# Optimization experiments

Measured on AMD Instinct MI355X. Metric: run time of the kernel, lower is better.

The kernel has to match this reference:

```python
import jax, jax.numpy as jnp
import numpy as np

B, S, D, L = 4, 4096, 2048, 4
QH, KVH, WINDOW = 16, 4, 512
HD = D // QH
G = QH // KVH
CAPF = 0.25
EPS = float(jnp.finfo(jnp.float32).eps)  # torch RMSNorm default eps for fp32


def setup_inputs() -> dict:
    key = jax.random.key(0)
    ks = jax.random.split(key, 8)
    s = 0.02
    return {
        "x": jax.random.normal(ks[0], (B, S, D), jnp.float32),
        "router_w": jax.random.normal(ks[1], (1, D), jnp.float32) * s,
        "norm1_w": jnp.ones((L, D), jnp.float32),
        "norm2_w": jnp.ones((L, D), jnp.float32),
        "qkv_w": jax.random.normal(ks[2], (L, (QH + 2 * KVH) * HD, D), jnp.float32) * s,
        "proj_w": jax.random.normal(ks[3], (L, D, D), jnp.float32) * s,
        "fc1_w": jax.random.normal(ks[4], (L, 2 * D, D), jnp.float32) * s,
        "fc2_w": jax.random.normal(ks[5], (L, D, D), jnp.float32) * s,
    }


def rmsnorm(x, w):
    return x * jax.lax.rsqrt(jnp.mean(x * x, -1, keepdims=True) + EPS) * w


def gqa(x, qkv_w, proj_w):
    # x: [B, C, D]; causal sliding-window attention with ALiBi (flash_attn semantics)
    b, c, _ = x.shape
    qkv = x @ qkv_w.T
    q = qkv[..., : QH * HD].reshape(b, c, KVH, G, HD)
    k = qkv[..., QH * HD:(QH + KVH) * HD].reshape(b, c, KVH, HD)
    v = qkv[..., (QH + KVH) * HD:].reshape(b, c, KVH, HD)
    scale = 1.0 / np.sqrt(HD)
    scores = jnp.einsum('bqkgd,bskd->bkgqs', q, k) * scale  # [B,KVH,G,C,C]
    i = jnp.arange(c)[:, None]
    j = jnp.arange(c)[None, :]
    diff = (i - j).astype(jnp.float32)
    mask = (diff >= 0) & (diff <= WINDOW)  # causal + left window
    slopes = jnp.exp2(-((jnp.arange(QH, dtype=jnp.float32) + 1.0) * 8.0 / QH))
    slopes = slopes.reshape(KVH, G, 1, 1)  # q head h = kvh*G + g ordering
    scores = jnp.where(mask, scores - slopes * diff, -jnp.inf)
    p = jax.nn.softmax(scores, axis=-1)
    att = jnp.einsum('bkgqs,bskd->bqkgd', p, v).reshape(b, c, QH * HD)
    return att @ proj_w.T


def swiglu(x, fc1_w, fc2_w):
    h = x @ fc1_w.T
    a, gate = jnp.split(h, 2, axis=-1)
    return (jax.nn.silu(gate) * a) @ fc2_w.T


def reference(x, router_w, norm1_w, norm2_w, qkv_w, proj_w, fc1_w, fc2_w):
    b, s, d = x.shape
    rw = jax.nn.sigmoid(x @ router_w.T)  # [B, S, 1]
    cap = int(s * CAPF)  # training path: capacity = int(seq_len * capacity_factor)
    rws = rw[..., 0]
    _, top_idx = jax.lax.top_k(rws, cap)            # unsorted-by-position top-k
    idx_sorted = jnp.sort(top_idx, axis=1)          # restore sequence order
    order = jnp.argsort(top_idx, axis=1)
    # faithful to source: gathers router_weights at the sort-order permutation
    # indices (values in [0, cap)), exactly as torch.gather(router_weights, 1, router_top_order)
    top_w = jnp.take_along_axis(rws, order, axis=1)[..., None]  # [B, cap, 1]
    lat = jnp.take_along_axis(x, idx_sorted[..., None], axis=1)  # [B, cap, D]
    for l in range(L):
        lat = lat + gqa(rmsnorm(lat, norm1_w[l]), qkv_w[l], proj_w[l])
        lat = lat + swiglu(rmsnorm(lat, norm2_w[l]), fc1_w[l], fc2_w[l])
    lat = lat * top_w
    bidx = jnp.arange(b)[:, None]
    pred = jnp.zeros_like(x).at[bidx, idx_sorted].set(lat)
    decisions = jnp.zeros_like(rw).at[bidx, idx_sorted].set(1.0)
    return pred, rw, decisions
```

## Files before the change

kernel.cpp:

```cpp
#include <hip/hip_runtime.h>
#include <hip/hip_bf16.h>

constexpr int NB = 4;
constexpr int SEQ = 4096;
constexpr int DIM = 2048;
constexpr int NLAYER = 4;
constexpr int NQH = 16;
constexpr int NKVH = 4;
constexpr int WIN = 512;
constexpr int HDIM = 128;
constexpr int CAPN = 1024;
constexpr int MTOK = NB * CAPN;
constexpr int QKVN = (NQH + 2 * NKVH) * HDIM;
constexpr int VOFF = DIM + NKVH * HDIM;
constexpr float EPSF = 1.1920928955078125e-07f;

typedef __hip_bfloat16 bf16;
typedef __bf16 b16x8 __attribute__((ext_vector_type(8)));
typedef __bf16 b16x4 __attribute__((ext_vector_type(4)));
typedef float f32x4 __attribute__((ext_vector_type(4)));

#define MFMA16(a, b, c) __builtin_amdgcn_mfma_f32_16x16x32_bf16((a), (b), (c), 0, 0, 0)

__device__ __forceinline__ void gload_lds16(const void* g, void* l) {
  __builtin_amdgcn_global_load_lds((__attribute__((address_space(1))) void*)(void*)g,
                                   (__attribute__((address_space(3))) void*)l, 16, 0, 0);
}

__global__ __launch_bounds__(256) void cast_kernel(const float* __restrict__ in,
                                                   bf16* __restrict__ out, int n) {
  int i = (blockIdx.x * 256 + threadIdx.x) * 4;
  if (i >= n) return;
  float4 v = *(const float4*)(in + i);
  b16x4 o;
  o[0] = (__bf16)v.x; o[1] = (__bf16)v.y; o[2] = (__bf16)v.z; o[3] = (__bf16)v.w;
  *(b16x4*)((__bf16*)out + i) = o;
}

__global__ __launch_bounds__(256) void cast_fc1_kernel(const float* __restrict__ in,
                                                       bf16* __restrict__ out) {
  int p = blockIdx.x;
  int chunk = p >> 5, w = p & 31;
  int L = (w < 16) ? (chunk * 16 + w) : (DIM + chunk * 16 + (w - 16));
  const float4* spv = (const float4*)(in + (size_t)L * DIM);
  __bf16* op = (__bf16*)out + (size_t)p * DIM;
  int t = threadIdx.x;
#pragma unroll
  for (int j = 0; j < 2; ++j) {
    float4 v = spv[t + j * 256];
    b16x4 o;
    o[0] = (__bf16)v.x; o[1] = (__bf16)v.y; o[2] = (__bf16)v.z; o[3] = (__bf16)v.w;
    *(b16x4*)(op + (t + j * 256) * 4) = o;
  }
}

__global__ __launch_bounds__(256) void router_kernel(const float* __restrict__ x,
                                                     const float* __restrict__ rwt,
                                                     float* __restrict__ rw_out) {
  int tok = blockIdx.x * 4 + (threadIdx.x >> 6);
  int l = threadIdx.x & 63;
  const float* xr = x + (size_t)tok * DIM;
  float s = 0.f;
  for (int c = l; c < DIM; c += 64) s += xr[c] * rwt[c];
  for (int off = 32; off; off >>= 1) s += __shfl_down(s, off);
  if (l == 0) rw_out[tok] = 1.f / (1.f + expf(-s));
}

__global__ __launch_bounds__(256) void rankcnt_kernel(const float* __restrict__ rw,
                                                      int* __restrict__ rank) {
  int blk = blockIdx.x;
  int ic = blk & 15, jc = (blk >> 4) & 15, b = blk >> 8;
  __shared__ float4 svi[64];
  int t = threadIdx.x;
  if (t < 64) svi[t] = ((const float4*)(rw + (size_t)b * SEQ + ic * 256))[t];
  __syncthreads();
  int j = jc * 256 + t;
  float vj = rw[(size_t)b * SEQ + j];
  int r = 0;
#pragma unroll 16
  for (int q = 0; q < 64; ++q) {
    float4 v = svi[q];
    int i = ic * 256 + q * 4;
    r += (v.x > vj || (v.x == vj && (i + 0) < j)) ? 1 : 0;
    r += (v.y > vj || (v.y == vj && (i + 1) < j)) ? 1 : 0;
    r += (v.z > vj || (v.z == vj && (i + 2) < j)) ? 1 : 0;
    r += (v.w > vj || (v.w == vj && (i + 3) < j)) ? 1 : 0;
  }
  atomicAdd(&rank[b * SEQ + j], r);
}

__global__ __launch_bounds__(1024) void select_kernel(const int* __restrict__ rank,
                                                      const float* __restrict__ rw,
                                                      int* __restrict__ idxs,
                                                      float* __restrict__ topw,
                                                      float* __restrict__ dec) {
  int b = blockIdx.x;
  int t = threadIdx.x;
  __shared__ int sr[SEQ];
  __shared__ int scnt[1024];
  for (int i = t; i < SEQ; i += 1024) sr[i] = rank[b * SEQ + i];
  __syncthreads();
  for (int i = t; i < SEQ; i += 1024) dec[(size_t)b * SEQ + i] = (sr[i] < CAPN) ? 1.0f : 0.0f;
  int c = 0;
#pragma unroll
  for (int k = 0; k < 4; ++k) c += (sr[t * 4 + k] < CAPN) ? 1 : 0;
  scnt[t] = c;
  __syncthreads();
  for (int off = 1; off < 1024; off <<= 1) {
    int v = scnt[t];
    int vm = (t >= off) ? scnt[t - off] : 0;
    __syncthreads();
    scnt[t] = v + vm;
    __syncthreads();
  }
  int pos = scnt[t] - c;
  for (int k = 0; k < 4; ++k) {
    int j = t * 4 + k;
    int r = sr[j];
    if (r < CAPN) {
      idxs[b * CAPN + pos] = j;
      topw[b * CAPN + pos] = rw[(size_t)b * SEQ + r];
      pos++;
    }
  }
}

__global__ __launch_bounds__(256) void gather_kernel(const float* __restrict__ x,
                                                     const int* __restrict__ idxs,
                                                     float* __restrict__ lat) {
  int tok = blockIdx.x;
  int b = tok >> 10, i = tok & 1023;
  int src = idxs[b * CAPN + i];
  const float4* spv = (const float4*)(x + ((size_t)b * SEQ + src) * DIM);
  float4* dp = (float4*)(lat + (size_t)tok * DIM);
  int t = threadIdx.x;
  dp[t] = spv[t];
  dp[t + 256] = spv[t + 256];
}

__global__ __launch_bounds__(256) void rmsnorm_kernel(const float* __restrict__ in,
                                                      const float* __restrict__ w,
                                                      bf16* __restrict__ out) {
  int row = blockIdx.x;
  int t = threadIdx.x;
  const float4* spv = (const float4*)(in + (size_t)row * DIM);
  float4 v0 = spv[t], v1 = spv[t + 256];
  float ss = v0.x * v0.x + v0.y * v0.y + v0.z * v0.z + v0.w * v0.w +
             v1.x * v1.x + v1.y * v1.y + v1.z * v1.z + v1.w * v1.w;
  for (int off = 32; off; off >>= 1) ss += __shfl_down(ss, off);
  __shared__ float red[4];
  if ((t & 63) == 0) red[t >> 6] = ss;
  __syncthreads();
  float total = red[0] + red[1] + red[2] + red[3];
  float sc = rsqrtf(total * (1.0f / DIM) + EPSF);
  const float4* wp = (const float4*)w;
  float4 w0 = wp[t], w1 = wp[t + 256];
  __bf16* op = (__bf16*)out + (size_t)row * DIM;
  b16x4 o0, o1;
  o0[0] = (__bf16)(v0.x * w0.x * sc); o0[1] = (__bf16)(v0.y * w0.y * sc);
  o0[2] = (__bf16)(v0.z * w0.z * sc); o0[3] = (__bf16)(v0.w * w0.w * sc);
  o1[0] = (__bf16)(v1.x * w1.x * sc); o1[1] = (__bf16)(v1.y * w1.y * sc);
  o1[2] = (__bf16)(v1.z * w1.z * sc); o1[3] = (__bf16)(v1.w * w1.w * sc);
  *(b16x4*)(op + t * 4) = o0;
  *(b16x4*)(op + 1024 + t * 4) = o1;
}


__device__ __forceinline__ void stage97(const bf16* g, int K, int kt,
                                        bf16* tile, int tid) {
#pragma unroll
  for (int j = 0; j < 4; ++j) {
    int q = j * 4096 + tid * 16;
    int row = q >> 7;
    int sc = ((tid & 7) ^ (row & 7)) << 3;
    gload_lds16((const __bf16*)g + (size_t)row * K + kt * 64 + sc,
                (char*)tile + q);
  }
}

__device__ __forceinline__ b16x8 frag97(const bf16* buf, int row, int ks, int hi) {
  int co = (ks * 32 + hi * 8) ^ ((row & 7) << 3);
  return *(const b16x8*)((const __bf16*)buf + row * 64 + co);
}

template <int MODE>
__global__ __launch_bounds__(256, 3) void gemm97(const bf16* __restrict__ A,
                                                 const bf16* __restrict__ Bw,
                                                 float* __restrict__ Cf,
                                                 bf16* __restrict__ Cb,
                                                 bf16* __restrict__ vTout,
                                                 int N, int K, int nbn) {
  __shared__ __align__(16) bf16 sA[128 * 64];
  __shared__ __align__(16) bf16 sB[128 * 64];
  const int tid = threadIdx.x;
  const int w = tid >> 6, l = tid & 63;
  const int lo = l & 15, hi = l >> 4;
  const int wr = w >> 1, wc = w & 1;
  const int nwg = gridDim.x;
  int bid = blockIdx.x;
  bid = (bid & 7) * (nwg >> 3) + (bid >> 3);
  const int bm = bid / nbn, bn = bid % nbn;
  const bf16* Ab = A + (size_t)bm * 128 * K;
  const bf16* Bb = Bw + (size_t)bn * 128 * K;
  const int nt = K >> 6;

  f32x4 acc[4][4];
#pragma unroll
  for (int i = 0; i < 4; ++i)
#pragma unroll
    for (int j = 0; j < 4; ++j) acc[i][j] = f32x4{0.f, 0.f, 0.f, 0.f};

  for (int t = 0; t < nt; ++t) {
    stage97(Ab, K, t, sA, tid);
    stage97(Bb, K, t, sB, tid);
    __syncthreads();
#pragma unroll
    for (int ks = 0; ks < 2; ++ks) {
      b16x8 af[4], bfm[4];
#pragma unroll
      for (int mi = 0; mi < 4; ++mi)
        af[mi] = frag97(sA, wr * 64 + mi * 16 + lo, ks, hi);
#pragma unroll
      for (int ni = 0; ni < 4; ++ni)
        bfm[ni] = frag97(sB, wc * 64 + ni * 16 + lo, ks, hi);
#pragma unroll
      for (int mi = 0; mi < 4; ++mi)
#pragma unroll
        for (int ni = 0; ni < 4; ++ni)
          acc[mi][ni] = MFMA16(af[mi], bfm[ni], acc[mi][ni]);
    }
    __syncthreads();
  }

#pragma unroll
  for (int mi = 0; mi < 4; ++mi) {
    int row0 = bm * 128 + wr * 64 + mi * 16 + hi * 4;
    if constexpr (MODE == 2) {
#pragma unroll
      for (int j2 = 0; j2 < 2; ++j2) {
        int colL = bn * 64 + wc * 32 + j2 * 16 + lo;
#pragma unroll
        for (int r = 0; r < 4; ++r) {
          float a = acc[mi][2 * j2][r];
          float g = acc[mi][2 * j2 + 1][r];
          float s = g / (1.f + __expf(-g));
          Cb[(size_t)(row0 + r) * DIM + colL] = __float2bfloat16(a * s);
        }
      }
    } else {
#pragma unroll
      for (int ni = 0; ni < 4; ++ni) {
        int col = bn * 128 + wc * 64 + ni * 16 + lo;
#pragma unroll
        for (int r = 0; r < 4; ++r) {
          size_t idx = (size_t)(row0 + r) * N + col;
          float v = acc[mi][ni][r];
          if constexpr (MODE == 3) {
            Cf[idx] += v;
          } else {
            bf16 bv = __float2bfloat16(v);
            Cb[idx] = bv;
            if constexpr (MODE == 1) {
              if (col >= VOFF) {
                int cc = col - VOFF;
                int kvh = cc >> 7, d = cc & 127;
                int row = row0 + r;
                int bb = row >> 10, tk = row & 1023;
                vTout[((size_t)(bb * NKVH + kvh) * HDIM + d) * CAPN + tk] = bv;
              }
            }
          }
        }
      }
    }
  }
}

__global__ __launch_bounds__(256) void attn_kernel(const bf16* __restrict__ qkvb,
                                                   const bf16* __restrict__ vT,
                                                   bf16* __restrict__ attb) {
  const int blk = blockIdx.x;
  const int qc = blk & 31;
  const int kvh = (blk >> 5) & 3;
  const int b = blk >> 7;
  const int w = threadIdx.x >> 6, l = threadIdx.x & 63;
  const int lo = l & 15, hi = l >> 4;
  const int h = kvh * 4 + w;
  const float slope = exp2f(-0.5f * (float)(h + 1));
  const float scale = 0.08838834764831845f;
  __shared__ __align__(16) bf16 p_lds[4][2][16 * 32];
  const __bf16* qp = (const __bf16*)qkvb;
  const __bf16* vtp = (const __bf16*)vT + (size_t)(b * NKVH + kvh) * HDIM * CAPN;
  const size_t tb = (size_t)b * CAPN;
  const int i0b = qc * 32;

  b16x8 aq[2][4];
#pragma unroll
  for (int qt = 0; qt < 2; ++qt) {
    const __bf16* qrow = qp + (tb + i0b + qt * 16 + lo) * QKVN + h * HDIM + hi * 8;
#pragma unroll
    for (int c = 0; c < 4; ++c) aq[qt][c] = *(const b16x8*)(qrow + c * 32);
  }

  f32x4 acc[2][8];
#pragma unroll
  for (int qt = 0; qt < 2; ++qt)
#pragma unroll
    for (int d = 0; d < 8; ++d) acc[qt][d] = f32x4{0.f, 0.f, 0.f, 0.f};
  float mrow[2][4], ssum[2][4];
#pragma unroll
  for (int qt = 0; qt < 2; ++qt)
#pragma unroll
    for (int r = 0; r < 4; ++r) { mrow[qt][r] = -1e30f; ssum[qt][r] = 0.f; }

  int jlo = i0b - WIN;
  if (jlo < 0) jlo = 0;
  jlo &= ~31;
  for (int j0 = jlo; j0 <= i0b; j0 += 32) {
    b16x8 kf[2][4];
#pragma unroll
    for (int jt = 0; jt < 2; ++jt) {
      const __bf16* krow = qp + (tb + j0 + jt * 16 + lo) * QKVN + DIM + kvh * HDIM + hi * 8;
#pragma unroll
      for (int c = 0; c < 4; ++c) kf[jt][c] = *(const b16x8*)(krow + c * 32);
    }
    f32x4 s[2][2];
#pragma unroll
    for (int qt = 0; qt < 2; ++qt)
#pragma unroll
      for (int jt = 0; jt < 2; ++jt) {
        s[qt][jt] = f32x4{0.f, 0.f, 0.f, 0.f};
#pragma unroll
        for (int c = 0; c < 4; ++c) s[qt][jt] = MFMA16(aq[qt][c], kf[jt][c], s[qt][jt]);
      }
#pragma unroll
    for (int qt = 0; qt < 2; ++qt) {
#pragma unroll
      for (int r = 0; r < 4; ++r) {
        const int i = i0b + qt * 16 + hi * 4 + r;
        float d0f = (float)(i - (j0 + lo));
        float d1f = (float)(i - (j0 + 16 + lo));
        float v0 = (d0f >= 0.f && d0f <= 512.f) ? (s[qt][0][r] * scale - slope * d0f) : -1e30f;
        float v1 = (d1f >= 0.f && d1f <= 512.f) ? (s[qt][1][r] * scale - slope * d1f) : -1e30f;
        float tm = fmaxf(v0, v1);
#pragma unroll
        for (int off = 1; off < 16; off <<= 1) tm = fmaxf(tm, __shfl_xor(tm, off));
        float mnew = fmaxf(mrow[qt][r], tm);
        float e0 = (v0 > -1e29f) ? __expf(v0 - mnew) : 0.f;
        float e1 = (v1 > -1e29f) ? __expf(v1 - mnew) : 0.f;
        float rs = e0 + e1;
#pragma unroll
        for (int off = 1; off < 16; off <<= 1) rs += __shfl_xor(rs, off);
        float corr = (mrow[qt][r] > -1e29f) ? __expf(mrow[qt][r] - mnew) : 0.f;
        ssum[qt][r] = ssum[qt][r] * corr + rs;
        mrow[qt][r] = mnew;
#pragma unroll
        for (int d = 0; d < 8; ++d) acc[qt][d][r] *= corr;
        p_lds[w][qt][(hi * 4 + r) * 32 + lo] = __float2bfloat16(e0);
        p_lds[w][qt][(hi * 4 + r) * 32 + 16 + lo] = __float2bfloat16(e1);
      }
    }
    b16x8 pa[2];
    pa[0] = *(const b16x8*)((const __bf16*)p_lds[w][0] + lo * 32 + hi * 8);
    pa[1] = *(const b16x8*)((const __bf16*)p_lds[w][1] + lo * 32 + hi * 8);
#pragma unroll
    for (int dh = 0; dh < 2; ++dh) {
      b16x8 bv[4];
#pragma unroll
      for (int dd = 0; dd < 4; ++dd) {
        int d = dh * 4 + dd;
        bv[dd] = *(const b16x8*)(vtp + (size_t)(d * 16 + lo) * CAPN + j0 + hi * 8);
      }
#pragma unroll
      for (int qt = 0; qt < 2; ++qt)
#pragma unroll
        for (int dd = 0; dd < 4; ++dd)
          acc[qt][dh * 4 + dd] = MFMA16(pa[qt], bv[dd], acc[qt][dh * 4 + dd]);
    }
  }
#pragma unroll
  for (int qt = 0; qt < 2; ++qt)
#pragma unroll
    for (int d = 0; d < 8; ++d)
#pragma unroll
      for (int r = 0; r < 4; ++r) {
        int row = i0b + qt * 16 + hi * 4 + r;
        attb[(tb + row) * DIM + h * HDIM + d * 16 + lo] =
            __float2bfloat16(acc[qt][d][r] / ssum[qt][r]);
      }
}

__global__ __launch_bounds__(256) void scatter_kernel(const float* __restrict__ lat,
                                                      const int* __restrict__ idxs,
                                                      const float* __restrict__ topw,
                                                      float* __restrict__ pred) {
  int tok = blockIdx.x;
  int b = tok >> 10, i = tok & 1023;
  int dst = idxs[b * CAPN + i];
  float wv = topw[b * CAPN + i];
  const float4* spv = (const float4*)(lat + (size_t)tok * DIM);
  float4* dp = (float4*)(pred + ((size_t)b * SEQ + dst) * DIM);
  int t = threadIdx.x;
  float4 v = spv[t];
  v.x *= wv; v.y *= wv; v.z *= wv; v.w *= wv;
  dp[t] = v;
  v = spv[t + 256];
  v.x *= wv; v.y *= wv; v.z *= wv; v.w *= wv;
  dp[t + 256] = v;
}

extern "C" void kernel_launch(void* const* d_in, const int* in_sizes, int n_in,
                              void* d_out, int out_size, void* d_ws, size_t ws_size,
                              hipStream_t stream) {
  const float* x        = (const float*)d_in[0];
  const float* router_w = (const float*)d_in[1];
  const float* norm1_w  = (const float*)d_in[2];
  const float* norm2_w  = (const float*)d_in[3];
  const float* qkv_w    = (const float*)d_in[4];
  const float* proj_w   = (const float*)d_in[5];
  const float* fc1_w    = (const float*)d_in[6];
  const float* fc2_w    = (const float*)d_in[7];

  float* pred   = (float*)d_out;
  float* rw_out = pred + (size_t)NB * SEQ * DIM;
  float* dec    = rw_out + (size_t)NB * SEQ;

  char* ws = (char*)d_ws;
  float* lat  = (float*)ws; ws += (size_t)MTOK * DIM * 4;
  bf16* xn    = (bf16*)ws;  ws += (size_t)MTOK * DIM * 2;
  bf16* qkvb  = (bf16*)ws;  ws += (size_t)MTOK * QKVN * 2;
  bf16* attb  = (bf16*)ws;  ws += (size_t)MTOK * DIM * 2;
  int* rank   = (int*)ws;   ws += (size_t)NB * SEQ * 4;
  int* idxs   = (int*)ws;   ws += (size_t)NB * CAPN * 4;
  float* topw = (float*)ws; ws += (size_t)NB * CAPN * 4;

  char* sp = (char*)pred;
  sp += (size_t)MTOK * (2 * DIM) * 2;
  bf16* wq = (bf16*)sp; sp += (size_t)QKVN * DIM * 2;
  bf16* wp = (bf16*)sp; sp += (size_t)DIM * DIM * 2;
  bf16* w1 = (bf16*)sp; sp += (size_t)(2 * DIM) * DIM * 2;
  bf16* w2 = (bf16*)sp; sp += (size_t)DIM * DIM * 2;
  bf16* vT = (bf16*)sp; sp += (size_t)NB * NKVH * HDIM * CAPN * 2;

  router_kernel<<<NB * SEQ / 4, 256, 0, stream>>>(x, router_w, rw_out);
  hipMemsetAsync(rank, 0, (size_t)NB * SEQ * 4, stream);
  rankcnt_kernel<<<NB * 256, 256, 0, stream>>>(rw_out, rank);
  select_kernel<<<NB, 1024, 0, stream>>>(rank, rw_out, idxs, topw, dec);
  gather_kernel<<<MTOK, 256, 0, stream>>>(x, idxs, lat);

  for (int l = 0; l < NLAYER; ++l) {
    cast_kernel<<<(QKVN * DIM) / 1024, 256, 0, stream>>>(qkv_w + (size_t)l * QKVN * DIM, wq, QKVN * DIM);
    cast_kernel<<<(DIM * DIM) / 1024, 256, 0, stream>>>(proj_w + (size_t)l * DIM * DIM, wp, DIM * DIM);
    cast_fc1_kernel<<<2 * DIM, 256, 0, stream>>>(fc1_w + (size_t)l * 2 * DIM * DIM, w1);
    cast_kernel<<<(DIM * DIM) / 1024, 256, 0, stream>>>(fc2_w + (size_t)l * DIM * DIM, w2, DIM * DIM);

    rmsnorm_kernel<<<MTOK, 256, 0, stream>>>(lat, norm1_w + (size_t)l * DIM, xn);
    gemm97<1><<<(MTOK / 128) * (QKVN / 128), 256, 0, stream>>>(
        xn, wq, nullptr, qkvb, vT, QKVN, DIM, QKVN / 128);
    attn_kernel<<<NB * NKVH * 32, 256, 0, stream>>>(qkvb, vT, attb);
    gemm97<3><<<(MTOK / 128) * (DIM / 128), 256, 0, stream>>>(
        attb, wp, lat, nullptr, nullptr, DIM, DIM, DIM / 128);

    rmsnorm_kernel<<<MTOK, 256, 0, stream>>>(lat, norm2_w + (size_t)l * DIM, xn);
    gemm97<2><<<(MTOK / 128) * (2 * DIM / 128), 256, 0, stream>>>(
        xn, w1, nullptr, attb, nullptr, 2 * DIM, DIM, 2 * DIM / 128);
    gemm97<3><<<(MTOK / 128) * (DIM / 128), 256, 0, stream>>>(
        attb, w2, lat, nullptr, nullptr, DIM, DIM, DIM / 128);
  }

  hipMemsetAsync(pred, 0, (size_t)NB * SEQ * DIM * 4, stream);
  scatter_kernel<<<MTOK, 256, 0, stream>>>(lat, idxs, topw, pred);
}
```

Baseline: 1.499 ms.

## Widen attention KV tiles to 64, iterate diagonal-first, use lazy softmax rescaling

The attention loop now processes 64 keys per iteration instead of 32 and walks from the diagonal tile backwards, so the running max is set early. It rescales the accumulators only when some row's max grows by more than a threshold, checked across the wavefront. The P tile in LDS is padded to a 72-element stride to reduce bank conflicts. The intent is fewer loop iterations, fewer exp and multiply rescale steps and better MFMA density, at the cost of more registers, some extra masked work at tile edges, and exponents up to e^8 when rescaling is skipped.

After: 1.498 ms. Within noise of the previous version (-0.1%).

```diff
diff --git a/kernel.cpp b/kernel.cpp
--- a/kernel.cpp
+++ b/kernel.cpp
@@ -288,7 +288,7 @@
   const int h = kvh * 4 + w;
   const float slope = exp2f(-0.5f * (float)(h + 1));
   const float scale = 0.08838834764831845f;
-  __shared__ __align__(16) bf16 p_lds[4][2][16 * 32];
+  __shared__ __align__(16) bf16 p_lds[4][2][16 * 72];
   const __bf16* qp = (const __bf16*)qkvb;
   const __bf16* vtp = (const __bf16*)vT + (size_t)(b * NKVH + kvh) * HDIM * CAPN;
   const size_t tb = (size_t)b * CAPN;
@@ -313,69 +313,100 @@
 #pragma unroll
     for (int r = 0; r < 4; ++r) { mrow[qt][r] = -1e30f; ssum[qt][r] = 0.f; }
 
-  int jlo = i0b - WIN;
-  if (jlo < 0) jlo = 0;
-  jlo &= ~31;
-  for (int j0 = jlo; j0 <= i0b; j0 += 32) {
-    b16x8 kf[2][4];
-#pragma unroll
-    for (int jt = 0; jt < 2; ++jt) {
+  const int Ttile = (i0b + 31) & ~63;
+  int Btile = i0b - WIN;
+  if (Btile < 0) Btile = 0;
+  Btile &= ~63;
+
+  for (int j0 = Ttile; j0 >= Btile; j0 -= 64) {
+    b16x8 kf[4][4];
+#pragma unroll
+    for (int jt = 0; jt < 4; ++jt) {
       const __bf16* krow = qp + (tb + j0 + jt * 16 + lo) * QKVN + DIM + kvh * HDIM + hi * 8;
 #pragma unroll
       for (int c = 0; c < 4; ++c) kf[jt][c] = *(const b16x8*)(krow + c * 32);
     }
-    f32x4 s[2][2];
+    f32x4 s[2][4];
 #pragma unroll
     for (int qt = 0; qt < 2; ++qt)
 #pragma unroll
-      for (int jt = 0; jt < 2; ++jt) {
+      for (int jt = 0; jt < 4; ++jt) {
         s[qt][jt] = f32x4{0.f, 0.f, 0.f, 0.f};
 #pragma unroll
         for (int c = 0; c < 4; ++c) s[qt][jt] = MFMA16(aq[qt][c], kf[jt][c], s[qt][jt]);
       }
+    float tmv[2][4];
+    int changed = 0;
 #pragma unroll
     for (int qt = 0; qt < 2; ++qt) {
 #pragma unroll
       for (int r = 0; r < 4; ++r) {
         const int i = i0b + qt * 16 + hi * 4 + r;
-        float d0f = (float)(i - (j0 + lo));
-        float d1f = (float)(i - (j0 + 16 + lo));
-        float v0 = (d0f >= 0.f && d0f <= 512.f) ? (s[qt][0][r] * scale - slope * d0f) : -1e30f;
-        float v1 = (d1f >= 0.f && d1f <= 512.f) ? (s[qt][1][r] * scale - slope * d1f) : -1e30f;
-        float tm = fmaxf(v0, v1);
+        float tm = -1e30f;
+#pragma unroll
+        for (int jt = 0; jt < 4; ++jt) {
+          int d = i - (j0 + jt * 16 + lo);
+          float v = (d >= 0 && d <= 512) ? (s[qt][jt][r] * scale - slope * (float)d)
+                                         : -1e30f;
+          s[qt][jt][r] = v;
+          tm = fmaxf(tm, v);
+        }
 #pragma unroll
         for (int off = 1; off < 16; off <<= 1) tm = fmaxf(tm, __shfl_xor(tm, off));
-        float mnew = fmaxf(mrow[qt][r], tm);
-        float e0 = (v0 > -1e29f) ? __expf(v0 - mnew) : 0.f;
-        float e1 = (v1 > -1e29f) ? __expf(v1 - mnew) : 0.f;
-        float rs = e0 + e1;
+        tmv[qt][r] = tm;
+        changed |= (tm > mrow[qt][r] + 8.0f) ? 1 : 0;
+      }
+    }
+    if (__any(changed)) {
+#pragma unroll
+      for (int qt = 0; qt < 2; ++qt)
+#pragma unroll
+        for (int r = 0; r < 4; ++r) {
+          float mnew = fmaxf(mrow[qt][r], tmv[qt][r]);
+          float corr = (mrow[qt][r] > -1e29f) ? __expf(mrow[qt][r] - mnew) : 0.f;
+          ssum[qt][r] *= corr;
+#pragma unroll
+          for (int d = 0; d < 8; ++d) acc[qt][d][r] *= corr;
+          mrow[qt][r] = mnew;
+        }
+    }
+#pragma unroll
+    for (int qt = 0; qt < 2; ++qt) {
+#pragma unroll
+      for (int r = 0; r < 4; ++r) {
+        const float m = mrow[qt][r];
+        float rs = 0.f;
+#pragma unroll
+        for (int jt = 0; jt < 4; ++jt) {
+          float v = s[qt][jt][r];
+          float p = (v > -1e29f) ? __expf(v - m) : 0.f;
+          rs += p;
+          p_lds[w][qt][(hi * 4 + r) * 72 + jt * 16 + lo] = __float2bfloat16(p);
+        }
 #pragma unroll
         for (int off = 1; off < 16; off <<= 1) rs += __shfl_xor(rs, off);
-        float corr = (mrow[qt][r] > -1e29f) ? __expf(mrow[qt][r] - mnew) : 0.f;
-        ssum[qt][r] = ssum[qt][r] * corr + rs;
-        mrow[qt][r] = mnew;
-#pragma unroll
-        for (int d = 0; d < 8; ++d) acc[qt][d][r] *= corr;
-        p_lds[w][qt][(hi * 4 + r) * 32 + lo] = __float2bfloat16(e0);
-        p_lds[w][qt][(hi * 4 + r) * 32 + 16 + lo] = __float2bfloat16(e1);
-      }
-    }
-    b16x8 pa[2];
-    pa[0] = *(const b16x8*)((const __bf16*)p_lds[w][0] + lo * 32 + hi * 8);
-    pa[1] = *(const b16x8*)((const __bf16*)p_lds[w][1] + lo * 32 + hi * 8);
-#pragma unroll
-    for (int dh = 0; dh < 2; ++dh) {
-      b16x8 bv[4];
-#pragma unroll
-      for (int dd = 0; dd < 4; ++dd) {
-        int d = dh * 4 + dd;
-        bv[dd] = *(const b16x8*)(vtp + (size_t)(d * 16 + lo) * CAPN + j0 + hi * 8);
-      }
-#pragma unroll
-      for (int qt = 0; qt < 2; ++qt)
-#pragma unroll
-        for (int dd = 0; dd < 4; ++dd)
-          acc[qt][dh * 4 + dd] = MFMA16(pa[qt], bv[dd], acc[qt][dh * 4 + dd]);
+        ssum[qt][r] += rs;
+      }
+    }
+#pragma unroll
+    for (int ks2 = 0; ks2 < 2; ++ks2) {
+      b16x8 pa[2];
+      pa[0] = *(const b16x8*)((const __bf16*)p_lds[w][0] + lo * 72 + ks2 * 32 + hi * 8);
+      pa[1] = *(const b16x8*)((const __bf16*)p_lds[w][1] + lo * 72 + ks2 * 32 + hi * 8);
+#pragma unroll
+      for (int dh = 0; dh < 2; ++dh) {
+        b16x8 bv[4];
+#pragma unroll
+        for (int dd = 0; dd < 4; ++dd) {
+          int d = dh * 4 + dd;
+          bv[dd] = *(const b16x8*)(vtp + (size_t)(d * 16 + lo) * CAPN + j0 + ks2 * 32 + hi * 8);
+        }
+#pragma unroll
+        for (int qt = 0; qt < 2; ++qt)
+#pragma unroll
+          for (int dd = 0; dd < 4; ++dd)
+            acc[qt][dh * 4 + dd] = MFMA16(pa[qt], bv[dd], acc[qt][dh * 4 + dd]);
+      }
     }
   }
 #pragma unroll
```
